# Kernel optimization log

Hardware: AMD Instinct MI355X
Metric: run time of the kernel (lower is better)

Reference implementation:

```python
import jax, jax.numpy as jnp
import numpy as np

TOP_K = 6
N_GROUP = 4
TOPK_GROUP = 2
ROUTED_SCALING = 2.5

T, H, E, I = 1024, 2048, 16, 704  # tokens, hidden, experts, expert ffn width
IS = 2 * I  # shared expert intermediate (n_shared_experts * moe_intermediate_size)


def setup_inputs() -> dict:
    key = jax.random.key(0)
    ks = jax.random.split(key, 6)
    s = 0.02
    return {
        "hidden_states": jax.random.normal(ks[0], (T, H), jnp.float32),
        "w_gate": jax.random.normal(ks[1], (H, E), jnp.float32) * s,
        "w_gate_up": jax.random.normal(ks[2], (E, H, 2 * I), jnp.float32) * s,
        "w_down": jax.random.normal(ks[3], (E, I, H), jnp.float32) * s,
        "w_shared_gate_up": jax.random.normal(ks[4], (H, 2 * IS), jnp.float32) * s,
        "w_shared_down": jax.random.normal(ks[5], (IS, H), jnp.float32) * s,
    }


def grouped_topk(scores, k, n_group, topk_group):
    # DeepSeek grouped top-k routing: pick topk_group expert groups by max
    # group score, mask out other groups, then top-k over remaining experts.
    t, e = scores.shape
    group_scores = scores.reshape(t, n_group, e // n_group).max(axis=-1)  # [T, G]
    _, gidx = jax.lax.top_k(group_scores, topk_group)                     # [T, kg]
    gmask = jax.nn.one_hot(gidx, n_group, dtype=scores.dtype).sum(axis=1)  # [T, G]
    smask = jnp.repeat(gmask, e // n_group, axis=1)                        # [T, E]
    masked = jnp.where(smask > 0, scores, 0.0)
    topk_w, topk_idx = jax.lax.top_k(masked, k)                            # [T, k]
    topk_w = topk_w / jnp.sum(topk_w, axis=-1, keepdims=True)              # renormalize
    return topk_w, topk_idx


def reference(hidden_states, w_gate, w_gate_up, w_down, w_shared_gate_up, w_shared_down):
    x = hidden_states                         # [T, H]
    t, e = x.shape[0], w_gate.shape[1]
    # router
    router_logits = x @ w_gate                # [T, E]
    scores = jax.nn.softmax(router_logits, axis=-1)
    topk_w, topk_idx = grouped_topk(scores, TOP_K, N_GROUP, TOPK_GROUP)
    combine = jnp.zeros((t, e), x.dtype).at[jnp.arange(t)[:, None], topk_idx].add(topk_w)
    # routed experts (dense-all-experts form, mathematically identical to dispatch)
    gu = jnp.einsum('th,ehi->tei', x, w_gate_up)        # [T, E, 2I]
    g, u = jnp.split(gu, 2, axis=-1)
    act = jax.nn.silu(g) * u                            # [T, E, I]
    act = act * combine[:, :, None]                     # apply routing weights
    routed = jnp.einsum('tei,eih->th', act, w_down) * ROUTED_SCALING
    # shared experts (SiLU gated MLP)
    sgu = x @ w_shared_gate_up
    sg, su = jnp.split(sgu, 2, axis=-1)
    shared = (jax.nn.silu(sg) * su) @ w_shared_down
    return routed + shared
```

## Files before the change

kernel.cpp:

```cpp
#include <hip/hip_runtime.h>

typedef unsigned short u16;
typedef u16 u16x8 __attribute__((ext_vector_type(8)));
typedef __bf16 bf16x8 __attribute__((ext_vector_type(8)));
typedef float f32x4 __attribute__((ext_vector_type(4)));
typedef unsigned u32x2 __attribute__((ext_vector_type(2)));

#define T_TOK 1024
#define H_DIM 2048
#define E_NUM 16
#define I_DIM 704
#define IS_DIM 1408

#define MFMA(a, b, c) __builtin_amdgcn_mfma_f32_16x16x32_bf16(a, b, c, 0, 0, 0)

__device__ __forceinline__ u16 f2bf(float f) {
  union { float f; unsigned u; } v; v.f = f;
  unsigned r = v.u + 0x7fffu + ((v.u >> 16) & 1u);
  return (u16)(r >> 16);
}

__device__ __forceinline__ void gload16(const void* g, void* l) {
  __builtin_amdgcn_global_load_lds(
      (const __attribute__((address_space(1))) unsigned int*)g,
      (__attribute__((address_space(3))) unsigned int*)l, 16, 0, 0);
}

__device__ __forceinline__ const char* lds_sw(const u16* base, int row, int kByte) {
  return (const char*)base + row * 128 + (kByte ^ ((row & 7) << 4));
}

__device__ __forceinline__ void transp_g_body(const float* __restrict__ in,
                                              u16* __restrict__ outp, int R, int C,
                                              int cx, int ry, int z, char* SM) {
  const size_t base = (size_t)z * (size_t)R * C;
  const int c0 = cx * 128, r0 = ry * 64;
  const int tid = threadIdx.x;
  const int w = tid >> 6;
#pragma unroll
  for (int j = 0; j < 8; ++j) {
    const int d = j * 256 + tid;
    const int row = d >> 5, cp = d & 31;
    const int c = cp ^ (row & 31);
    gload16(in + base + (size_t)(r0 + row) * C + c0 + c * 4,
            SM + (size_t)(j * 256 + w * 64) * 16);
  }
  __syncthreads();
#pragma unroll
  for (int i = 0; i < 8; ++i) {
    const int idx = i * 256 + tid;
    const int oc = idx >> 4, pp = idx & 15;
    float f[4];
#pragma unroll
    for (int k = 0; k < 4; ++k) {
      const int r = 4 * pp + k;
      f[k] = *(const float*)(SM + r * 512 + ((((oc >> 2) ^ (r & 31)) << 4)) +
                             (oc & 3) * 4);
    }
    u32x2 wv;
    wv[0] = (unsigned)f2bf(f[0]) | ((unsigned)f2bf(f[1]) << 16);
    wv[1] = (unsigned)f2bf(f[2]) | ((unsigned)f2bf(f[3]) << 16);
    *(u32x2*)&outp[base + (size_t)(c0 + oc) * R + r0 + 4 * pp] = wv;
  }
}

__device__ __forceinline__ void router_body(const float* __restrict__ x,
                                            const float* __restrict__ wg,
                                            float* __restrict__ comb,
                                            u16* __restrict__ XB, int t, char* SM) {
  const int tid = threadIdx.x;
  const float* xr = x + (size_t)t * H_DIM;
  const int h0 = tid * 8;
  f32x4 a = *(const f32x4*)(xr + h0);
  f32x4 b = *(const f32x4*)(xr + h0 + 4);
  u16x8 o;
  o[0] = f2bf(a[0]); o[1] = f2bf(a[1]); o[2] = f2bf(a[2]); o[3] = f2bf(a[3]);
  o[4] = f2bf(b[0]); o[5] = f2bf(b[1]); o[6] = f2bf(b[2]); o[7] = f2bf(b[3]);
  *(u16x8*)(XB + (size_t)t * H_DIM + h0) = o;

  float acc[E_NUM];
#pragma unroll
  for (int e = 0; e < E_NUM; ++e) acc[e] = 0.f;
#pragma unroll
  for (int j = 0; j < 8; ++j) {
    const float xv = j < 4 ? a[j] : b[j - 4];
    const f32x4* wr = (const f32x4*)(wg + (size_t)(h0 + j) * E_NUM);
#pragma unroll
    for (int q = 0; q < 4; ++q) {
      f32x4 w4 = wr[q];
      acc[q * 4 + 0] += xv * w4[0];
      acc[q * 4 + 1] += xv * w4[1];
      acc[q * 4 + 2] += xv * w4[2];
      acc[q * 4 + 3] += xv * w4[3];
    }
  }
#pragma unroll
  for (int e = 0; e < E_NUM; ++e)
    for (int off = 32; off > 0; off >>= 1) acc[e] += __shfl_down(acc[e], off);
  float (*part)[E_NUM] = (float(*)[E_NUM])SM;
  if ((tid & 63) == 0) {
#pragma unroll
    for (int e = 0; e < E_NUM; ++e) part[tid >> 6][e] = acc[e];
  }
  __syncthreads();
  if (tid == 0) {
    float p[E_NUM];
    float mx = -1e30f;
    for (int e = 0; e < E_NUM; ++e) {
      p[e] = part[0][e] + part[1][e] + part[2][e] + part[3][e];
      mx = fmaxf(mx, p[e]);
    }
    float s = 0.f;
    for (int e = 0; e < E_NUM; ++e) { p[e] = __expf(p[e] - mx); s += p[e]; }
    const float invs = 1.f / s;
    for (int e = 0; e < E_NUM; ++e) p[e] *= invs;
    float gs[4];
    for (int g = 0; g < 4; ++g)
      gs[g] = fmaxf(fmaxf(p[4 * g], p[4 * g + 1]), fmaxf(p[4 * g + 2], p[4 * g + 3]));
    int g1 = 0;
    for (int g = 1; g < 4; ++g) if (gs[g] > gs[g1]) g1 = g;
    int g2 = -1;
    for (int g = 0; g < 4; ++g) {
      if (g == g1) continue;
      if (g2 < 0 || gs[g] > gs[g2]) g2 = g;
    }
    float m2[E_NUM], cw[E_NUM];
    for (int e = 0; e < E_NUM; ++e) {
      int g = e >> 2;
      m2[e] = (g == g1 || g == g2) ? p[e] : 0.f;
      cw[e] = 0.f;
    }
    float sum6 = 0.f;
    for (int k = 0; k < 6; ++k) {
      int bi = 0; float bv = -1.f;
      for (int e = 0; e < E_NUM; ++e)
        if (m2[e] > bv) { bv = m2[e]; bi = e; }
      cw[bi] = bv; sum6 += bv; m2[bi] = -2.f;
    }
    const float scale = 2.5f / sum6;
    for (int e = 0; e < E_NUM; ++e) comb[t * E_NUM + e] = cw[e] * scale;
  }
}

#define FP_ROUTER T_TOK
#define FP_ZERO 512
#define FP_WGU (11 * 32 * 16)
#define FP_WSGU (22 * 32)
__global__ __launch_bounds__(256) void fused_pre_k(
    const float* __restrict__ x, const float* __restrict__ wg,
    float* __restrict__ comb, u16* __restrict__ XB,
    const float* __restrict__ wgu, const float* __restrict__ wsgu,
    u16* __restrict__ WGUT, u16* __restrict__ WSGUT, float* __restrict__ outz) {
  __shared__ __align__(16) char SM[32768];
  const int bid = blockIdx.x;
  if (bid < FP_ROUTER) {
    router_body(x, wg, comb, XB, bid, SM);
  } else if (bid < FP_ROUTER + FP_ZERO) {
    const int i = ((bid - FP_ROUTER) * 256 + threadIdx.x) * 16;
    const f32x4 z = {0.f, 0.f, 0.f, 0.f};
#pragma unroll
    for (int j = 0; j < 4; ++j) *(f32x4*)(outz + i + j * 4) = z;
  } else if (bid < FP_ROUTER + FP_ZERO + FP_WGU) {
    const int id = bid - FP_ROUTER - FP_ZERO;
    transp_g_body(wgu, WGUT, H_DIM, 2 * I_DIM, id % 11, (id / 11) % 32,
                  id / 352, SM);
  } else {
    const int id = bid - FP_ROUTER - FP_ZERO - FP_WGU;
    transp_g_body(wsgu, WSGUT, H_DIM, 2 * IS_DIM, id % 22, id / 22, 0, SM);
  }
}

__global__ __launch_bounds__(256) void dispatch_k(const float* __restrict__ comb,
                                                  int* __restrict__ cnt,
                                                  int* __restrict__ tok) {
  const int e = blockIdx.x;
  const int tid = threadIdx.x;
  const int lane = tid & 63, wid = tid >> 6;
  __shared__ int wtot[4];
  int running = 0;
  for (int chunk = 0; chunk < T_TOK / 256; ++chunk) {
    const int t = chunk * 256 + tid;
    const bool sel = comb[t * E_NUM + e] > 0.f;
    unsigned long long mask = __ballot(sel);
    const int pre = __popcll(mask & ((1ull << lane) - 1ull));
    if (lane == 0) wtot[wid] = __popcll(mask);
    __syncthreads();
    int wbase = running;
    for (int w = 0; w < wid; ++w) wbase += wtot[w];
    if (sel) tok[e * T_TOK + wbase + pre] = t;
    running += wtot[0] + wtot[1] + wtot[2] + wtot[3];
    __syncthreads();
  }
  if (tid == 0) cnt[e] = running;
}

__device__ __forceinline__ void gu_body(
    const u16* __restrict__ A, const u16* __restrict__ Bt,
    const float* __restrict__ comb, const int* __restrict__ cnt,
    const int* __restrict__ tok, u16* __restrict__ outp,
    int gu_off, long long bt_e_stride, long long out_e_stride, int out_stride,
    int bx, int by, int e, char* SM) {
  const int M = cnt ? cnt[e] : T_TOK;
  const int m0 = by * 128;
  if (m0 >= M) return;
  u16* S = (u16*)SM;

  const int n0 = bx * 64;
  const u16* Bte = Bt + (size_t)e * bt_e_stride;
  const u16* Bgp = Bte + (size_t)n0 * H_DIM;
  const u16* Bup = Bte + (size_t)(gu_off + n0) * H_DIM;
  const int tid = threadIdx.x;
  const int w = tid >> 6, l = tid & 63;
  const int r8 = l >> 3;
  const int sk = ((l & 7) ^ r8) * 8;

  size_t arow[4];
#pragma unroll
  for (int j = 0; j < 4; ++j) {
    const int m = m0 + w * 32 + j * 8 + r8;
    const int mc = m < M ? m : M - 1;
    const int t = tok ? tok[e * T_TOK + mc] : mc;
    arow[j] = (size_t)t * H_DIM + sk;
  }

  const int wr = tid >> 7;
  const int wc = (tid >> 6) & 1;
  const int fr = l & 15;
  const int fg = l >> 4;

  const f32x4 zero = {0.f, 0.f, 0.f, 0.f};
  f32x4 accg[4][2], accu[4][2];
#pragma unroll
  for (int i = 0; i < 4; ++i)
#pragma unroll
    for (int j = 0; j < 2; ++j) { accg[i][j] = zero; accu[i][j] = zero; }

  for (int kt = 0; kt < H_DIM / 64; ++kt) {
    const int k0 = kt * 64;
#pragma unroll
    for (int j = 0; j < 4; ++j)
      gload16(A + arow[j] + k0, S + (w * 4 + j) * 512);
#pragma unroll
    for (int j = 0; j < 2; ++j) {
      const size_t br = (size_t)(w * 16 + j * 8 + r8) * H_DIM + sk + k0;
      gload16(Bgp + br, S + 8192 + (w * 2 + j) * 512);
      gload16(Bup + br, S + 12288 + (w * 2 + j) * 512);
    }
    __syncthreads();
    const u16* AsC = S;
    const u16* BgC = S + 8192;
    const u16* BuC = S + 12288;
#pragma unroll
    for (int kk = 0; kk < 2; ++kk) {
      const int kb = kk * 64 + fg * 16;
      bf16x8 af[4], bg[2], bu[2];
#pragma unroll
      for (int mi = 0; mi < 4; ++mi)
        af[mi] = *(const bf16x8*)lds_sw(AsC, wr * 64 + mi * 16 + fr, kb);
#pragma unroll
      for (int ni = 0; ni < 2; ++ni) {
        bg[ni] = *(const bf16x8*)lds_sw(BgC, wc * 32 + ni * 16 + fr, kb);
        bu[ni] = *(const bf16x8*)lds_sw(BuC, wc * 32 + ni * 16 + fr, kb);
      }
#pragma unroll
      for (int mi = 0; mi < 4; ++mi)
#pragma unroll
        for (int ni = 0; ni < 2; ++ni) {
          accg[mi][ni] = MFMA(af[mi], bg[ni], accg[mi][ni]);
          accu[mi][ni] = MFMA(af[mi], bu[ni], accu[mi][ni]);
        }
    }
    __syncthreads();
  }

  const int colb = n0 + wc * 32;
#pragma unroll
  for (int mi = 0; mi < 4; ++mi) {
#pragma unroll
    for (int r = 0; r < 4; ++r) {
      const int ml = wr * 64 + mi * 16 + fg * 4 + r;
      if (m0 + ml >= M) continue;
      const int trow = tok ? tok[e * T_TOK + m0 + ml] : (m0 + ml);
      const float wgt = comb ? comb[trow * E_NUM + e] : 1.0f;
      const size_t rowoff = (size_t)e * out_e_stride + (size_t)(m0 + ml) * out_stride;
#pragma unroll
      for (int ni = 0; ni < 2; ++ni) {
        float g = accg[mi][ni][r];
        float u = accu[mi][ni][r];
        float sg = g / (1.f + __expf(-g));
        outp[rowoff + colb + ni * 16 + fr] = f2bf(sg * u * wgt);
      }
    }
  }
}

#define MG_GUR_BLKS (11 * 8 * 16)
#define MG_GUS_BLKS (22 * 8)
#define MG_TWD_BLKS (16 * 11 * 16)
#define MG_TWSD_BLKS (16 * 22)
__global__ __launch_bounds__(256, 4) void mega_k(
    const u16* __restrict__ XB, const u16* __restrict__ WGUT,
    const u16* __restrict__ WSGUT, const float* __restrict__ comb,
    const int* __restrict__ cnt, const int* __restrict__ tok,
    u16* __restrict__ ACTC, u16* __restrict__ ACTS,
    const float* __restrict__ wd, const float* __restrict__ wsd,
    u16* __restrict__ WDT, u16* __restrict__ WSDT) {
  __shared__ __align__(16) char SM[32768];
  const int bid = blockIdx.x;
  if (bid < MG_GUR_BLKS) {
    gu_body(XB, WGUT, comb, cnt, tok, ACTC, I_DIM, (long long)(2 * I_DIM) * H_DIM,
            (long long)T_TOK * I_DIM, I_DIM, bid % 11, (bid / 11) % 8, bid / 88, SM);
  } else if (bid < MG_GUR_BLKS + MG_GUS_BLKS) {
    const int id = bid - MG_GUR_BLKS;
    gu_body(XB, WSGUT, nullptr, nullptr, nullptr, ACTS, IS_DIM, 0, 0, IS_DIM,
            id % 22, id / 22, 0, SM);
  } else if (bid < MG_GUR_BLKS + MG_GUS_BLKS + MG_TWD_BLKS) {
    const int id = bid - MG_GUR_BLKS - MG_GUS_BLKS;
    transp_g_body(wd, WDT, I_DIM, H_DIM, id % 16, (id / 16) % 11, id / 176, SM);
  } else {
    const int id = bid - MG_GUR_BLKS - MG_GUS_BLKS - MG_TWD_BLKS;
    transp_g_body(wsd, WSDT, IS_DIM, H_DIM, id % 16, id / 16, 0, SM);
  }
}

__device__ __forceinline__ void down_core_atomic(
    const u16* __restrict__ Ap, int astride,
    const u16* __restrict__ Bp, int bstride,
    int NT, int M, int m0, int n0, const int* tokS, float* __restrict__ outp) {
  __shared__ __align__(16) u16 S[12288];
  const int tid = threadIdx.x;
  const int w = tid >> 6, l = tid & 63;
  const int r8 = l >> 3;
  const int sk = ((l & 7) ^ r8) * 8;

  size_t arow[2];
#pragma unroll
  for (int j = 0; j < 2; ++j) {
    const int m = w * 16 + j * 8 + r8;
    arow[j] = (size_t)(m0 + m < M ? m : (M - 1 - m0 > 0 ? M - 1 - m0 : 0)) * astride + sk;
  }
  size_t brow[4];
#pragma unroll
  for (int j = 0; j < 4; ++j)
    brow[j] = (size_t)(w * 32 + j * 8 + r8) * bstride + sk;

  const int fr = l & 15, fg = l >> 4;
  const f32x4 zero = {0.f, 0.f, 0.f, 0.f};
  f32x4 acc[4][2];
#pragma unroll
  for (int i = 0; i < 4; ++i)
#pragma unroll
    for (int j = 0; j < 2; ++j) acc[i][j] = zero;

  for (int kt = 0; kt < NT; ++kt) {
    const int k0 = kt * 64;
#pragma unroll
    for (int j = 0; j < 2; ++j)
      gload16(Ap + arow[j] + k0, S + (w * 2 + j) * 512);
#pragma unroll
    for (int j = 0; j < 4; ++j)
      gload16(Bp + brow[j] + k0, S + 4096 + (w * 4 + j) * 512);
    __syncthreads();
    const u16* AsC = S;
    const u16* BsC = S + 4096;
#pragma unroll
    for (int kk = 0; kk < 2; ++kk) {
      const int kb = kk * 64 + fg * 16;
      bf16x8 af[4], bfr[2];
#pragma unroll
      for (int mi = 0; mi < 4; ++mi)
        af[mi] = *(const bf16x8*)lds_sw(AsC, mi * 16 + fr, kb);
#pragma unroll
      for (int ni = 0; ni < 2; ++ni)
        bfr[ni] = *(const bf16x8*)lds_sw(BsC, w * 32 + ni * 16 + fr, kb);
#pragma unroll
      for (int mi = 0; mi < 4; ++mi)
#pragma unroll
        for (int ni = 0; ni < 2; ++ni) acc[mi][ni] = MFMA(af[mi], bfr[ni], acc[mi][ni]);
    }
    __syncthreads();
  }

#pragma unroll
  for (int mi = 0; mi < 4; ++mi) {
#pragma unroll
    for (int r = 0; r < 4; ++r) {
      const int ml = mi * 16 + fg * 4 + r;
      if (m0 + ml >= M) continue;
      float* op = outp + (size_t)tokS[ml] * H_DIM + n0 + w * 32;
#pragma unroll
      for (int ni = 0; ni < 2; ++ni)
        atomicAdd(op + ni * 16 + fr, acc[mi][ni][r]);
    }
  }
}

__global__ __launch_bounds__(256, 4) void down_all_k(
    const u16* __restrict__ ACTC, const u16* __restrict__ WDT,
    const u16* __restrict__ ACTS, const u16* __restrict__ WSDT,
    const int* __restrict__ cnt, const int* __restrict__ tok,
    float* __restrict__ outp) {
  const int e = blockIdx.z;
  const bool shared = (e == E_NUM);
  const int M = shared ? T_TOK : cnt[e];
  const int m0 = blockIdx.y * 64;
  if (m0 >= M) return;
  const int n0 = blockIdx.x * 128;
  __shared__ int tokS[64];
  const int tid = threadIdx.x;
  if (tid < 64) {
    const int m = m0 + tid;
    tokS[tid] = shared ? m : tok[e * T_TOK + (m < M ? m : M - 1)];
  }
  __syncthreads();
  if (shared)
    down_core_atomic(ACTS + (size_t)m0 * IS_DIM, IS_DIM,
                     WSDT + (size_t)n0 * IS_DIM, IS_DIM,
                     IS_DIM / 64, M, m0, n0, tokS, outp);
  else
    down_core_atomic(ACTC + ((size_t)e * T_TOK + m0) * I_DIM, I_DIM,
                     WDT + ((size_t)e * H_DIM + n0) * I_DIM, I_DIM,
                     I_DIM / 64, M, m0, n0, tokS, outp);
}

extern "C" void kernel_launch(void* const* d_in, const int* in_sizes, int n_in,
                              void* d_out, int out_size, void* d_ws, size_t ws_size,
                              hipStream_t stream) {
  const float* x    = (const float*)d_in[0];
  const float* wg   = (const float*)d_in[1];
  const float* wgu  = (const float*)d_in[2];
  const float* wd   = (const float*)d_in[3];
  const float* wsgu = (const float*)d_in[4];
  const float* wsd  = (const float*)d_in[5];
  float* out = (float*)d_out;

  char* ws = (char*)d_ws;
  size_t off = 0;
  auto alloc = [&](size_t b) { size_t r = off; off += (b + 255) & ~(size_t)255; return r; };
  u16*   XB    = (u16*)  (ws + alloc((size_t)T_TOK * H_DIM * 2));
  float* COMB  = (float*)(ws + alloc((size_t)T_TOK * E_NUM * 4));
  int*   CNT   = (int*)  (ws + alloc((size_t)E_NUM * 4));
  int*   TOK   = (int*)  (ws + alloc((size_t)E_NUM * T_TOK * 4));
  u16*   WGUT  = (u16*)  (ws + alloc((size_t)E_NUM * 2 * I_DIM * H_DIM * 2));
  u16*   WDT   = (u16*)  (ws + alloc((size_t)E_NUM * H_DIM * I_DIM * 2));
  u16*   WSGUT = (u16*)  (ws + alloc((size_t)2 * IS_DIM * H_DIM * 2));
  u16*   WSDT  = (u16*)  (ws + alloc((size_t)H_DIM * IS_DIM * 2));
  u16*   ACTC  = (u16*)  (ws + alloc((size_t)E_NUM * T_TOK * I_DIM * 2));
  u16*   ACTS  = (u16*)  (ws + alloc((size_t)T_TOK * IS_DIM * 2));
  if (ws_size < off) return;

  fused_pre_k<<<FP_ROUTER + FP_ZERO + FP_WGU + FP_WSGU, 256, 0, stream>>>(
      x, wg, COMB, XB, wgu, wsgu, WGUT, WSGUT, out);
  dispatch_k<<<E_NUM, 256, 0, stream>>>(COMB, CNT, TOK);
  mega_k<<<MG_GUR_BLKS + MG_GUS_BLKS + MG_TWD_BLKS + MG_TWSD_BLKS, 256, 0, stream>>>(
      XB, WGUT, WSGUT, COMB, CNT, TOK, ACTC, ACTS, wd, wsd, WDT, WSDT);
  down_all_k<<<dim3(H_DIM / 128, T_TOK / 64, E_NUM + 1), 256, 0, stream>>>(
      ACTC, WDT, ACTS, WSDT, CNT, TOK, out);
}
```

Before: 249.3 us.

## Store transposed bf16 weights in contiguous 64x64 tiles for GEMM loads

The transpose kernels now write the bf16 weights as contiguous 64x64 tiles (8 KB each), ordered by output-column tile then K tile, instead of plain row-major transposed matrices. The gate/up and down GEMM loaders index these tiles, so each K step reads one contiguous 8 KB block per B operand rather than 64 rows spread H_DIM or I_DIM elements apart. This is meant to improve DRAM and TLB locality for the weight streams. The transpose writes become scattered per tile, and every consumer has to agree on the tile indexing.

```diff
diff --git a/kernel.cpp b/kernel.cpp
--- a/kernel.cpp
+++ b/kernel.cpp
@@ -30,10 +30,9 @@
   return (const char*)base + row * 128 + (kByte ^ ((row & 7) << 4));
 }
 
-__device__ __forceinline__ void transp_g_body(const float* __restrict__ in,
-                                              u16* __restrict__ outp, int R, int C,
-                                              int cx, int ry, int z, char* SM) {
-  const size_t base = (size_t)z * (size_t)R * C;
+__device__ __forceinline__ void transp_tile_body(const float* __restrict__ in_e,
+                                                 u16* __restrict__ out_e, int Cn,
+                                                 int NTK, int cx, int ry, char* SM) {
   const int c0 = cx * 128, r0 = ry * 64;
   const int tid = threadIdx.x;
   const int w = tid >> 6;
@@ -42,7 +41,7 @@
     const int d = j * 256 + tid;
     const int row = d >> 5, cp = d & 31;
     const int c = cp ^ (row & 31);
-    gload16(in + base + (size_t)(r0 + row) * C + c0 + c * 4,
+    gload16(in_e + (size_t)(r0 + row) * Cn + c0 + c * 4,
             SM + (size_t)(j * 256 + w * 64) * 16);
   }
   __syncthreads();
@@ -60,7 +59,8 @@
     u32x2 wv;
     wv[0] = (unsigned)f2bf(f[0]) | ((unsigned)f2bf(f[1]) << 16);
     wv[1] = (unsigned)f2bf(f[2]) | ((unsigned)f2bf(f[3]) << 16);
-    *(u32x2*)&outp[base + (size_t)(c0 + oc) * R + r0 + 4 * pp] = wv;
+    const size_t tbase = (size_t)(((c0 >> 6) + (oc >> 6)) * NTK + ry) * 4096;
+    *(u32x2*)&out_e[tbase + (oc & 63) * 64 + 4 * pp] = wv;
   }
 }
 
@@ -162,11 +162,13 @@
     for (int j = 0; j < 4; ++j) *(f32x4*)(outz + i + j * 4) = z;
   } else if (bid < FP_ROUTER + FP_ZERO + FP_WGU) {
     const int id = bid - FP_ROUTER - FP_ZERO;
-    transp_g_body(wgu, WGUT, H_DIM, 2 * I_DIM, id % 11, (id / 11) % 32,
-                  id / 352, SM);
+    const int e = id / 352;
+    transp_tile_body(wgu + (size_t)e * H_DIM * 2 * I_DIM,
+                     WGUT + (size_t)e * 2 * I_DIM * H_DIM, 2 * I_DIM, 32,
+                     id % 11, (id / 11) % 32, SM);
   } else {
     const int id = bid - FP_ROUTER - FP_ZERO - FP_WGU;
-    transp_g_body(wsgu, WSGUT, H_DIM, 2 * IS_DIM, id % 22, id / 22, 0, SM);
+    transp_tile_body(wsgu, WSGUT, 2 * IS_DIM, 32, id % 22, id / 22, SM);
   }
 }
 
@@ -198,7 +200,7 @@
     const u16* __restrict__ A, const u16* __restrict__ Bt,
     const float* __restrict__ comb, const int* __restrict__ cnt,
     const int* __restrict__ tok, u16* __restrict__ outp,
-    int gu_off, long long bt_e_stride, long long out_e_stride, int out_stride,
+    int gu_off_t, long long bt_e_stride, long long out_e_stride, int out_stride,
     int bx, int by, int e, char* SM) {
   const int M = cnt ? cnt[e] : T_TOK;
   const int m0 = by * 128;
@@ -207,8 +209,8 @@
 
   const int n0 = bx * 64;
   const u16* Bte = Bt + (size_t)e * bt_e_stride;
-  const u16* Bgp = Bte + (size_t)n0 * H_DIM;
-  const u16* Bup = Bte + (size_t)(gu_off + n0) * H_DIM;
+  const u16* Bgp = Bte + (size_t)((n0 >> 6) * 32) * 4096;
+  const u16* Bup = Bte + (size_t)((gu_off_t + (n0 >> 6)) * 32) * 4096;
   const int tid = threadIdx.x;
   const int w = tid >> 6, l = tid & 63;
   const int r8 = l >> 3;
@@ -222,6 +224,7 @@
     const int t = tok ? tok[e * T_TOK + mc] : mc;
     arow[j] = (size_t)t * H_DIM + sk;
   }
+  const int browoff[2] = {(w * 16 + 0 + r8) * 64 + sk, (w * 16 + 8 + r8) * 64 + sk};
 
   const int wr = tid >> 7;
   const int wc = (tid >> 6) & 1;
@@ -237,14 +240,14 @@
 
   for (int kt = 0; kt < H_DIM / 64; ++kt) {
     const int k0 = kt * 64;
+    const int tb = kt * 4096;
 #pragma unroll
     for (int j = 0; j < 4; ++j)
       gload16(A + arow[j] + k0, S + (w * 4 + j) * 512);
 #pragma unroll
     for (int j = 0; j < 2; ++j) {
-      const size_t br = (size_t)(w * 16 + j * 8 + r8) * H_DIM + sk + k0;
-      gload16(Bgp + br, S + 8192 + (w * 2 + j) * 512);
-      gload16(Bup + br, S + 12288 + (w * 2 + j) * 512);
+      gload16(Bgp + tb + browoff[j], S + 8192 + (w * 2 + j) * 512);
+      gload16(Bup + tb + browoff[j], S + 12288 + (w * 2 + j) * 512);
     }
     __syncthreads();
     const u16* AsC = S;
@@ -308,24 +311,27 @@
   __shared__ __align__(16) char SM[32768];
   const int bid = blockIdx.x;
   if (bid < MG_GUR_BLKS) {
-    gu_body(XB, WGUT, comb, cnt, tok, ACTC, I_DIM, (long long)(2 * I_DIM) * H_DIM,
-            (long long)T_TOK * I_DIM, I_DIM, bid % 11, (bid / 11) % 8, bid / 88, SM);
+    gu_body(XB, WGUT, comb, cnt, tok, ACTC, I_DIM / 64,
+            (long long)(2 * I_DIM) * H_DIM, (long long)T_TOK * I_DIM, I_DIM,
+            bid % 11, (bid / 11) % 8, bid / 88, SM);
   } else if (bid < MG_GUR_BLKS + MG_GUS_BLKS) {
     const int id = bid - MG_GUR_BLKS;
-    gu_body(XB, WSGUT, nullptr, nullptr, nullptr, ACTS, IS_DIM, 0, 0, IS_DIM,
+    gu_body(XB, WSGUT, nullptr, nullptr, nullptr, ACTS, IS_DIM / 64, 0, 0, IS_DIM,
             id % 22, id / 22, 0, SM);
   } else if (bid < MG_GUR_BLKS + MG_GUS_BLKS + MG_TWD_BLKS) {
     const int id = bid - MG_GUR_BLKS - MG_GUS_BLKS;
-    transp_g_body(wd, WDT, I_DIM, H_DIM, id % 16, (id / 16) % 11, id / 176, SM);
+    const int e = id / 176;
+    transp_tile_body(wd + (size_t)e * I_DIM * H_DIM,
+                     WDT + (size_t)e * H_DIM * I_DIM, H_DIM, 11,
+                     id % 16, (id / 16) % 11, SM);
   } else {
     const int id = bid - MG_GUR_BLKS - MG_GUS_BLKS - MG_TWD_BLKS;
-    transp_g_body(wsd, WSDT, IS_DIM, H_DIM, id % 16, id / 16, 0, SM);
+    transp_tile_body(wsd, WSDT, H_DIM, 22, id % 16, id / 16, SM);
   }
 }
 
 __device__ __forceinline__ void down_core_atomic(
-    const u16* __restrict__ Ap, int astride,
-    const u16* __restrict__ Bp, int bstride,
+    const u16* __restrict__ Ap, int astride, const u16* __restrict__ Bp, int NTK,
     int NT, int M, int m0, int n0, const int* tokS, float* __restrict__ outp) {
   __shared__ __align__(16) u16 S[12288];
   const int tid = threadIdx.x;
@@ -341,8 +347,10 @@
   }
   size_t brow[4];
 #pragma unroll
-  for (int j = 0; j < 4; ++j)
-    brow[j] = (size_t)(w * 32 + j * 8 + r8) * bstride + sk;
+  for (int j = 0; j < 4; ++j) {
+    const int row = w * 32 + j * 8 + r8;
+    brow[j] = (size_t)((row >> 6) * NTK) * 4096 + (row & 63) * 64 + sk;
+  }
 
   const int fr = l & 15, fg = l >> 4;
   const f32x4 zero = {0.f, 0.f, 0.f, 0.f};
@@ -354,12 +362,13 @@
 
   for (int kt = 0; kt < NT; ++kt) {
     const int k0 = kt * 64;
+    const int tb = kt * 4096;
 #pragma unroll
     for (int j = 0; j < 2; ++j)
       gload16(Ap + arow[j] + k0, S + (w * 2 + j) * 512);
 #pragma unroll
     for (int j = 0; j < 4; ++j)
-      gload16(Bp + brow[j] + k0, S + 4096 + (w * 4 + j) * 512);
+      gload16(Bp + brow[j] + tb, S + 4096 + (w * 4 + j) * 512);
     __syncthreads();
     const u16* AsC = S;
     const u16* BsC = S + 4096;
@@ -415,11 +424,12 @@
   __syncthreads();
   if (shared)
     down_core_atomic(ACTS + (size_t)m0 * IS_DIM, IS_DIM,
-                     WSDT + (size_t)n0 * IS_DIM, IS_DIM,
+                     WSDT + (size_t)((n0 >> 6) * 22) * 4096, 22,
                      IS_DIM / 64, M, m0, n0, tokS, outp);
   else
     down_core_atomic(ACTC + ((size_t)e * T_TOK + m0) * I_DIM, I_DIM,
-                     WDT + ((size_t)e * H_DIM + n0) * I_DIM, I_DIM,
+                     WDT + (size_t)e * H_DIM * I_DIM +
+                         (size_t)((n0 >> 6) * 11) * 4096, 11,
                      I_DIM / 64, M, m0, n0, tokS, outp);
 }
 
```

Measured after the change: 247.0 us. No clear change (-0.9%).
